# Optimization experiments

Measured on AMD Instinct MI355X. Metric: run time of the kernel, lower is better.

## Reference

```python
import jax, jax.numpy as jnp
import numpy as np

N = 50000      # nodes
E = 800000     # edges
IN = 128       # in_feats
NH = 128       # n_hidden (per-head out_feats)
H = 2          # num_heads
P = 100000     # node pairs for the head MLP
C = 2          # n_classes
NEG_SLOPE = 0.2


def setup_inputs() -> dict:
    key = jax.random.key(0)
    ks = jax.random.split(key, 16)
    def glorot(k, shape, fan_in):
        return jax.random.normal(k, shape, jnp.float32) * (1.0 / np.sqrt(fan_in))
    return {
        "src": jax.random.randint(ks[0], (E,), 0, N),
        "dst": jax.random.randint(ks[1], (E,), 0, N),
        "h": jax.random.normal(ks[2], (N, IN), jnp.float32),
        "x1": jax.random.randint(ks[3], (P,), 0, N),
        "x2": jax.random.randint(ks[4], (P,), 0, N),
        # GATConv layer 0
        "W0": glorot(ks[5], (IN, H * NH), IN),
        "al0": glorot(ks[6], (H, NH), NH),
        "ar0": glorot(ks[7], (H, NH), NH),
        # GATConv layer 1
        "W1": glorot(ks[8], (NH, H * NH), NH),
        "al1": glorot(ks[9], (H, NH), NH),
        "ar1": glorot(ks[10], (H, NH), NH),
        # head MLP (weights stored as [in, out])
        "w1": glorot(ks[11], (3 * NH, NH), 3 * NH),
        "b1": jnp.zeros((NH,), jnp.float32),
        "w2": glorot(ks[12], (NH, C), NH),
        "b2": jnp.zeros((C,), jnp.float32),
    }


def gat_conv(h, src, dst, W, al, ar):
    # h: [N, d_in] -> feat: [N, H, F]
    feat = (h @ W).reshape(h.shape[0], H, -1)
    el = jnp.einsum("nhf,hf->nh", feat, al)  # [N, H]
    er = jnp.einsum("nhf,hf->nh", feat, ar)  # [N, H]
    e = jax.nn.leaky_relu(el[src] + er[dst], NEG_SLOPE)  # [E, H]
    # edge softmax segmented by destination node
    emax = jax.ops.segment_max(e, dst, num_segments=N)
    ee = jnp.exp(e - emax[dst])
    denom = jax.ops.segment_sum(ee, dst, num_segments=N)
    alpha = ee / (denom[dst] + 1e-9)                      # [E, H]
    msg = feat[src] * alpha[..., None]                    # [E, H, F]
    out = jax.ops.segment_sum(msg, dst, num_segments=N)   # [N, H, F]
    return jax.nn.relu(out)


def reference(src, dst, h, x1, x2, W0, al0, ar0, W1, al1, ar1, w1, b1, w2, b2):
    h = gat_conv(h, src, dst, W0, al0, ar0).mean(axis=1)  # [N, NH]
    h = gat_conv(h, src, dst, W1, al1, ar1).mean(axis=1)  # [N, NH]
    h1, h2 = h[x1], h[x2]                                 # [P, NH]
    z = jnp.concatenate([h1, h2, jnp.abs(h1 - h2)], axis=1)
    z = jax.nn.relu(z @ w1 + b1)
    return z @ w2 + b2                                    # [P, C]
```

## Files before the change

### kernel.cpp

```cpp
#include <hip/hip_runtime.h>
#include <hip/hip_bf16.h>

#define NN 50000
#define NE 800000
#define NPAIR 100000

typedef unsigned int u32;
typedef unsigned short u16;
typedef __attribute__((ext_vector_type(8))) short short8;
typedef __attribute__((ext_vector_type(4))) float f32x4;

__device__ __forceinline__ float bflo(u32 u) { return __uint_as_float(u << 16); }
__device__ __forceinline__ float bfhi(u32 u) { return __uint_as_float(u & 0xffff0000u); }
__device__ __forceinline__ u32 bfround(float f) {
    u32 u = __float_as_uint(f);
    return (u + 0x7fffu + ((u >> 16) & 1u)) >> 16;
}
__device__ __forceinline__ u32 packbf(float a, float b) {
    return bfround(a) | (bfround(b) << 16);
}

__global__ __launch_bounds__(256) void count_kernel(const int* __restrict__ dst, int* __restrict__ off) {
    int e = blockIdx.x * 256 + threadIdx.x;
    if (e < NE) atomicAdd(&off[dst[e] + 1], 1);
}

__global__ __launch_bounds__(256) void scan1(int* __restrict__ data, int* __restrict__ bsums, int n) {
    int tid = threadIdx.x;
    int i = blockIdx.x * 256 + tid;
    int v = (i < n) ? data[i] : 0;
    #pragma unroll
    for (int d = 1; d < 64; d <<= 1) {
        int t = __shfl_up(v, d);
        if ((tid & 63) >= d) v += t;
    }
    __shared__ int ws[4];
    if ((tid & 63) == 63) ws[tid >> 6] = v;
    __syncthreads();
    int w = tid >> 6;
    if (w > 0) v += ws[0];
    if (w > 1) v += ws[1];
    if (w > 2) v += ws[2];
    if (i < n) data[i] = v;
    if (tid == 255) bsums[blockIdx.x] = v;
}

__global__ __launch_bounds__(256) void scan2(int* __restrict__ bsums, int nb) {
    int tid = threadIdx.x;
    int v = (tid < nb) ? bsums[tid] : 0;
    #pragma unroll
    for (int d = 1; d < 64; d <<= 1) {
        int t = __shfl_up(v, d);
        if ((tid & 63) >= d) v += t;
    }
    __shared__ int ws[4];
    if ((tid & 63) == 63) ws[tid >> 6] = v;
    __syncthreads();
    int w = tid >> 6;
    if (w > 0) v += ws[0];
    if (w > 1) v += ws[1];
    if (w > 2) v += ws[2];
    if (tid < nb) bsums[tid] = v;
}

__global__ __launch_bounds__(256) void scan3(int* __restrict__ data, const int* __restrict__ bsums, int n) {
    int i = blockIdx.x * 256 + threadIdx.x;
    if (i < n && blockIdx.x > 0) data[i] += bsums[blockIdx.x - 1];
}

__global__ __launch_bounds__(256) void fill_kernel(const int* __restrict__ src, const int* __restrict__ dst,
                                                   const int* __restrict__ off,
                                                   int* __restrict__ cursor, int* __restrict__ srcs) {
    int e = blockIdx.x * 256 + threadIdx.x;
    if (e < NE) {
        int d = dst[e];
        int pos = off[d] + atomicAdd(&cursor[d], 1);
        srcs[pos] = src[e];
    }
}

__global__ __launch_bounds__(256) void pack_all(const float* __restrict__ W0, const float* __restrict__ W1,
                                                const float* __restrict__ w1,
                                                u16* __restrict__ w0pg, u16* __restrict__ w1pg,
                                                u16* __restrict__ w1p) {
    int id = blockIdx.x * 256 + threadIdx.x;
    if (id < 65536) {
        const float* W = (id < 32768) ? W0 : W1;
        u16* Wp = (id < 32768) ? w0pg : w1pg;
        int t = id & 32767;
        int k = t >> 8, n = t & 255;
        int kt = k >> 5, kk = k & 31, lg = kk >> 3, j = kk & 7;
        int nt = n >> 4, ln = n & 15;
        int lane = lg * 16 + ln;
        Wp[(((kt * 16 + nt) * 64) + lane) * 8 + j] = (u16)bfround(W[t]);
    } else if (id < 65536 + 49152) {
        int t = id - 65536;
        int k = t >> 7, n = t & 127;
        int kt = k >> 5, kk = k & 31, lg = kk >> 3, j = kk & 7;
        int ct = n >> 4, ln = n & 15;
        int lane = lg * 16 + ln;
        w1p[(((kt * 8 + ct) * 64) + lane) * 8 + j] = (u16)bfround(w1[t]);
    }
}

template<bool ABF16>
__global__ __launch_bounds__(256) void gemm_mfma(const void* __restrict__ Av,
                                                 const u16* __restrict__ Wp,
                                                 const float* __restrict__ al,
                                                 const float* __restrict__ ar,
                                                 u16* __restrict__ C,
                                                 float* __restrict__ att, int nrows) {
    __shared__ u16 sbuf[64 * 264];
    int rbase = blockIdx.x * 64;
    int tid = threadIdx.x;
    if (ABF16) {
        const uint4* A4 = (const uint4*)Av;
        for (int id = tid; id < 64 * 16; id += 256) {
            int r = id >> 4, seg = id & 15;
            int gr = rbase + r;
            uint4 v = make_uint4(0u, 0u, 0u, 0u);
            if (gr < nrows) v = A4[gr * 16 + seg];
            *(uint4*)&sbuf[r * 136 + seg * 8] = v;
        }
    } else {
        const float4* A4 = (const float4*)Av;
        for (int id = tid; id < 64 * 32; id += 256) {
            int r = id >> 5, seg = id & 31;
            int gr = rbase + r;
            float4 v = make_float4(0.f, 0.f, 0.f, 0.f);
            if (gr < nrows) v = A4[gr * 32 + seg];
            uint2 p;
            p.x = packbf(v.x, v.y);
            p.y = packbf(v.z, v.w);
            *(uint2*)&sbuf[r * 136 + seg * 4] = p;
        }
    }
    __syncthreads();
    int l = tid & 63, w = tid >> 6;
    int ln = l & 15, lg = l >> 4;
    f32x4 acc[16];
    #pragma unroll
    for (int nt = 0; nt < 16; ++nt) acc[nt] = (f32x4){0.f, 0.f, 0.f, 0.f};
    const short8* wp = (const short8*)Wp;
    const u16* arow = &sbuf[(w * 16 + ln) * 136 + lg * 8];
    #pragma unroll
    for (int kt = 0; kt < 4; ++kt) {
        short8 a = *(const short8*)&arow[kt * 32];
        #pragma unroll
        for (int nt = 0; nt < 16; ++nt) {
            short8 b = wp[(kt * 16 + nt) * 64 + l];
            acc[nt] = __builtin_amdgcn_mfma_f32_16x16x32_bf16(a, b, acc[nt], 0, 0, 0);
        }
    }
    float alv[16], arv[16];
    #pragma unroll
    for (int nt = 0; nt < 16; ++nt) {
        alv[nt] = al[nt * 16 + ln];
        arv[nt] = ar[nt * 16 + ln];
    }
    #pragma unroll
    for (int r = 0; r < 4; ++r) {
        float pl0 = 0.f, pr0 = 0.f, pl1 = 0.f, pr1 = 0.f;
        #pragma unroll
        for (int nt = 0; nt < 8; ++nt) {
            pl0 += acc[nt][r] * alv[nt];
            pr0 += acc[nt][r] * arv[nt];
            pl1 += acc[nt + 8][r] * alv[nt + 8];
            pr1 += acc[nt + 8][r] * arv[nt + 8];
        }
        #pragma unroll
        for (int m = 1; m < 16; m <<= 1) {
            pl0 += __shfl_xor(pl0, m); pr0 += __shfl_xor(pr0, m);
            pl1 += __shfl_xor(pl1, m); pr1 += __shfl_xor(pr1, m);
        }
        int grow = rbase + w * 16 + lg * 4 + r;
        if (ln == 0 && grow < nrows) {
            att[grow * 4 + 0] = pl0;
            att[grow * 4 + 1] = pl1;
            att[grow * 4 + 2] = pr0;
            att[grow * 4 + 3] = pr1;
        }
    }
    __syncthreads();
    #pragma unroll
    for (int nt = 0; nt < 16; ++nt) {
        int col = nt * 16 + ln;
        #pragma unroll
        for (int r = 0; r < 4; ++r) {
            int row = w * 16 + lg * 4 + r;
            sbuf[row * 264 + col] = (u16)bfround(acc[nt][r]);
        }
    }
    __syncthreads();
    uint4* C4 = (uint4*)C;
    for (int id = tid; id < 64 * 32; id += 256) {
        int r = id >> 5, seg = id & 31;
        int gr = rbase + r;
        if (gr < nrows) C4[gr * 32 + seg] = *(uint4*)&sbuf[r * 264 + seg * 8];
    }
}

__global__ __launch_bounds__(128) void aggregate(const u16* __restrict__ feat,
                                                 const int* __restrict__ off,
                                                 const int* __restrict__ srcs,
                                                 const float* __restrict__ att,
                                                 u16* __restrict__ hout) {
    int v = blockIdx.x * 2 + (threadIdx.x >> 6);
    int lane = threadIdx.x & 63;
    if (v >= NN) return;
    int s = off[v], deg = off[v + 1] - s;
    const float4* att4 = (const float4*)att;
    const uint2* featu2 = (const uint2*)feat;
    uint2* houtu2 = (uint2*)hout;
    float4 av = att4[v];
    float er0 = av.z, er1 = av.w;
    bool h0 = lane < 32;
    float m0 = -1e30f, m1 = -1e30f, d0 = 0.f, d1 = 0.f;
    float a0 = 0.f, a1 = 0.f, a2 = 0.f, a3 = 0.f;
    for (int cb = 0; cb < deg; cb += 64) {
        int k = cb + lane;
        int cn = min(64, deg - cb);
        int u = 0;
        float e0 = -1e30f, e1 = -1e30f;
        if (k < deg) {
            u = srcs[s + k];
            float4 au = att4[u];
            e0 = au.x + er0; e0 = e0 > 0.f ? e0 : 0.2f * e0;
            e1 = au.y + er1; e1 = e1 > 0.f ? e1 : 0.2f * e1;
        }
        float mc0 = e0, mc1 = e1;
        #pragma unroll
        for (int mm = 1; mm < 64; mm <<= 1) {
            mc0 = fmaxf(mc0, __shfl_xor(mc0, mm));
            mc1 = fmaxf(mc1, __shfl_xor(mc1, mm));
        }
        float m0n = fmaxf(m0, mc0), m1n = fmaxf(m1, mc1);
        float f0 = __expf(m0 - m0n), f1 = __expf(m1 - m1n);
        float w0 = (k < deg) ? __expf(e0 - m0n) : 0.f;
        float w1 = (k < deg) ? __expf(e1 - m1n) : 0.f;
        float s0 = w0, s1 = w1;
        #pragma unroll
        for (int mm = 1; mm < 64; mm <<= 1) {
            s0 += __shfl_xor(s0, mm);
            s1 += __shfl_xor(s1, mm);
        }
        d0 = d0 * f0 + s0;
        d1 = d1 * f1 + s1;
        float fa = h0 ? f0 : f1;
        a0 *= fa; a1 *= fa; a2 *= fa; a3 *= fa;
        m0 = m0n; m1 = m1n;
        int k2 = 0;
        for (; k2 + 4 <= cn; k2 += 4) {
            int uu0 = __shfl(u, k2), uu1 = __shfl(u, k2 + 1);
            int uu2 = __shfl(u, k2 + 2), uu3 = __shfl(u, k2 + 3);
            float wa0 = __shfl(w0, k2), wb0 = __shfl(w1, k2);
            float wa1 = __shfl(w0, k2 + 1), wb1 = __shfl(w1, k2 + 1);
            float wa2 = __shfl(w0, k2 + 2), wb2 = __shfl(w1, k2 + 2);
            float wa3 = __shfl(w0, k2 + 3), wb3 = __shfl(w1, k2 + 3);
            float wk0 = h0 ? wa0 : wb0, wk1 = h0 ? wa1 : wb1;
            float wk2 = h0 ? wa2 : wb2, wk3 = h0 ? wa3 : wb3;
            uint2 g0 = featu2[(size_t)uu0 * 64 + lane];
            uint2 g1 = featu2[(size_t)uu1 * 64 + lane];
            uint2 g2 = featu2[(size_t)uu2 * 64 + lane];
            uint2 g3 = featu2[(size_t)uu3 * 64 + lane];
            a0 += wk0 * bflo(g0.x) + wk1 * bflo(g1.x) + wk2 * bflo(g2.x) + wk3 * bflo(g3.x);
            a1 += wk0 * bfhi(g0.x) + wk1 * bfhi(g1.x) + wk2 * bfhi(g2.x) + wk3 * bfhi(g3.x);
            a2 += wk0 * bflo(g0.y) + wk1 * bflo(g1.y) + wk2 * bflo(g2.y) + wk3 * bflo(g3.y);
            a3 += wk0 * bfhi(g0.y) + wk1 * bfhi(g1.y) + wk2 * bfhi(g2.y) + wk3 * bfhi(g3.y);
        }
        for (; k2 < cn; ++k2) {
            int uu = __shfl(u, k2);
            float wa = __shfl(w0, k2), wb = __shfl(w1, k2);
            float wk = h0 ? wa : wb;
            uint2 g = featu2[(size_t)uu * 64 + lane];
            a0 += wk * bflo(g.x); a1 += wk * bfhi(g.x);
            a2 += wk * bflo(g.y); a3 += wk * bfhi(g.y);
        }
    }
    float dh = h0 ? d0 : d1;
    float r = 1.f / (dh + 1e-9f);
    float o0 = fmaxf(a0 * r, 0.f), o1 = fmaxf(a1 * r, 0.f);
    float o2 = fmaxf(a2 * r, 0.f), o3 = fmaxf(a3 * r, 0.f);
    float p0 = __shfl_xor(o0, 32), p1 = __shfl_xor(o1, 32);
    float p2 = __shfl_xor(o2, 32), p3 = __shfl_xor(o3, 32);
    if (h0) {
        uint2 q;
        q.x = packbf(0.5f * (o0 + p0), 0.5f * (o1 + p1));
        q.y = packbf(0.5f * (o2 + p2), 0.5f * (o3 + p3));
        houtu2[(size_t)v * 32 + lane] = q;
    }
}

__global__ __launch_bounds__(256) void mlp_mfma(const u16* __restrict__ hf,
                                                const int* __restrict__ x1,
                                                const int* __restrict__ x2,
                                                const u16* __restrict__ w1p,
                                                const float* __restrict__ b1,
                                                const float* __restrict__ w2,
                                                const float* __restrict__ b2,
                                                float* __restrict__ out) {
    __shared__ u16 z[64][392];
    int pbase = blockIdx.x * 64;
    int tid = threadIdx.x;
    const uint4* hfu4 = (const uint4*)hf;
    for (int id = tid; id < 64 * 16; id += 256) {
        int p = id >> 4, seg = id & 15;
        int gp = pbase + p;
        uint4 v1 = make_uint4(0u, 0u, 0u, 0u), v2 = v1;
        if (gp < NPAIR) {
            v1 = hfu4[x1[gp] * 16 + seg];
            v2 = hfu4[x2[gp] * 16 + seg];
        }
        int c8 = seg << 3;
        *(uint4*)&z[p][c8] = v1;
        *(uint4*)&z[p][128 + c8] = v2;
        uint4 vd;
        vd.x = packbf(fabsf(bflo(v1.x) - bflo(v2.x)), fabsf(bfhi(v1.x) - bfhi(v2.x)));
        vd.y = packbf(fabsf(bflo(v1.y) - bflo(v2.y)), fabsf(bfhi(v1.y) - bfhi(v2.y)));
        vd.z = packbf(fabsf(bflo(v1.z) - bflo(v2.z)), fabsf(bfhi(v1.z) - bfhi(v2.z)));
        vd.w = packbf(fabsf(bflo(v1.w) - bflo(v2.w)), fabsf(bfhi(v1.w) - bfhi(v2.w)));
        *(uint4*)&z[p][256 + c8] = vd;
    }
    __syncthreads();
    int l = tid & 63, w = tid >> 6;
    int lg = l >> 4, ln = l & 15;
    f32x4 acc[8];
    #pragma unroll
    for (int ct = 0; ct < 8; ++ct) acc[ct] = (f32x4){0.f, 0.f, 0.f, 0.f};
    const short8* wp = (const short8*)w1p;
    const u16* zr = &z[w * 16 + ln][lg * 8];
    for (int kt = 0; kt < 12; ++kt) {
        short8 a = *(const short8*)&zr[kt * 32];
        #pragma unroll
        for (int ct = 0; ct < 8; ++ct) {
            short8 b = wp[(kt * 8 + ct) * 64 + l];
            acc[ct] = __builtin_amdgcn_mfma_f32_16x16x32_bf16(a, b, acc[ct], 0, 0, 0);
        }
    }
    float b1v[8], w20[8], w21[8];
    #pragma unroll
    for (int ct = 0; ct < 8; ++ct) {
        int n = ct * 16 + ln;
        b1v[ct] = b1[n];
        w20[ct] = w2[n * 2 + 0];
        w21[ct] = w2[n * 2 + 1];
    }
    float ob0 = b2[0], ob1 = b2[1];
    #pragma unroll
    for (int r = 0; r < 4; ++r) {
        float p0 = 0.f, p1 = 0.f;
        #pragma unroll
        for (int ct = 0; ct < 8; ++ct) {
            float zv = fmaxf(acc[ct][r] + b1v[ct], 0.f);
            p0 += zv * w20[ct]; p1 += zv * w21[ct];
        }
        #pragma unroll
        for (int m = 1; m < 16; m <<= 1) { p0 += __shfl_xor(p0, m); p1 += __shfl_xor(p1, m); }
        int gp = pbase + w * 16 + lg * 4 + r;
        if (ln == 0 && gp < NPAIR) {
            out[gp * 2 + 0] = p0 + ob0;
            out[gp * 2 + 1] = p1 + ob1;
        }
    }
}

extern "C" void kernel_launch(void* const* d_in, const int* in_sizes, int n_in,
                              void* d_out, int out_size, void* d_ws, size_t ws_size,
                              hipStream_t stream) {
    const int*   src = (const int*)d_in[0];
    const int*   dst = (const int*)d_in[1];
    const float* h   = (const float*)d_in[2];
    const int*   x1  = (const int*)d_in[3];
    const int*   x2  = (const int*)d_in[4];
    const float* W0  = (const float*)d_in[5];
    const float* al0 = (const float*)d_in[6];
    const float* ar0 = (const float*)d_in[7];
    const float* W1  = (const float*)d_in[8];
    const float* al1 = (const float*)d_in[9];
    const float* ar1 = (const float*)d_in[10];
    const float* w1  = (const float*)d_in[11];
    const float* b1  = (const float*)d_in[12];
    const float* w2  = (const float*)d_in[13];
    const float* b2  = (const float*)d_in[14];
    float* out = (float*)d_out;

    char* ws = (char*)d_ws;
    size_t o = 0;
    auto alloc = [&](size_t bytes) { size_t r = o; o = (o + bytes + 255) & ~255UL; return r; };
    int* off    = (int*)(ws + alloc((NN + 1) * sizeof(int)));
    int* cursor = (int*)(ws + alloc(NN * sizeof(int)));
    int* bsums  = (int*)(ws + alloc(256 * sizeof(int)));
    int* srcs   = (int*)(ws + alloc(NE * sizeof(int)));
    float* att  = (float*)(ws + alloc((size_t)NN * 4 * sizeof(float)));
    u16* feat   = (u16*)(ws + alloc((size_t)NN * 256 * sizeof(u16)));
    u16* hb0    = (u16*)(ws + alloc((size_t)NN * 128 * sizeof(u16)));
    u16* hb1    = (u16*)(ws + alloc((size_t)NN * 128 * sizeof(u16)));
    u16* w1p    = (u16*)(ws + alloc((size_t)384 * 128 * sizeof(u16)));
    u16* w0pg   = (u16*)(ws + alloc((size_t)128 * 256 * sizeof(u16)));
    u16* w1pg   = (u16*)(ws + alloc((size_t)128 * 256 * sizeof(u16)));

    hipMemsetAsync(off, 0, (NN + 1) * sizeof(int), stream);
    hipMemsetAsync(cursor, 0, NN * sizeof(int), stream);

    int eblocks = (NE + 255) / 256;
    int nscan = NN + 1;
    int nb = (nscan + 255) / 256;
    count_kernel<<<eblocks, 256, 0, stream>>>(dst, off);
    scan1<<<nb, 256, 0, stream>>>(off, bsums, nscan);
    scan2<<<1, 256, 0, stream>>>(bsums, nb);
    scan3<<<nb, 256, 0, stream>>>(off, bsums, nscan);
    fill_kernel<<<eblocks, 256, 0, stream>>>(src, dst, off, cursor, srcs);
    pack_all<<<448, 256, 0, stream>>>(W0, W1, w1, w0pg, w1pg, w1p);

    int gblocks = (NN + 63) / 64;
    gemm_mfma<false><<<gblocks, 256, 0, stream>>>((const void*)h, w0pg, al0, ar0, feat, att, NN);
    aggregate<<<(NN + 1) / 2, 128, 0, stream>>>(feat, off, srcs, att, hb0);
    gemm_mfma<true><<<gblocks, 256, 0, stream>>>((const void*)hb0, w1pg, al1, ar1, feat, att, NN);
    aggregate<<<(NN + 1) / 2, 128, 0, stream>>>(feat, off, srcs, att, hb1);
    mlp_mfma<<<(NPAIR + 63) / 64, 256, 0, stream>>>(hb1, x1, x2, w1p, b1, w2, b2, out);
}
```

Measured before the change: 383.2 us.

## Widen aggregate gathers to 16-byte loads with two edges per wavefront step

The aggregation kernel now has each lane load a uint4 (8 bf16 values) instead of a uint2. The two half-waves each handle a different edge, so one wavefront gathers two neighbor rows per step, and the partial sums are combined with a cross-half shuffle at the end. The block size doubles to 256 threads (4 nodes per block), and zero-degree nodes take an early-exit path. The aim is fewer, wider memory instructions and more edges in flight per wave, at the cost of extra accumulator registers and a final shuffle reduction.

```diff
diff --git a/kernel.cpp b/kernel.cpp
--- a/kernel.cpp
+++ b/kernel.cpp
@@ -200,23 +200,30 @@
     }
 }
 
-__global__ __launch_bounds__(128) void aggregate(const u16* __restrict__ feat,
+__global__ __launch_bounds__(256) void aggregate(const u16* __restrict__ feat,
                                                  const int* __restrict__ off,
                                                  const int* __restrict__ srcs,
                                                  const float* __restrict__ att,
                                                  u16* __restrict__ hout) {
-    int v = blockIdx.x * 2 + (threadIdx.x >> 6);
+    int v = blockIdx.x * 4 + (threadIdx.x >> 6);
     int lane = threadIdx.x & 63;
     if (v >= NN) return;
     int s = off[v], deg = off[v + 1] - s;
     const float4* att4 = (const float4*)att;
-    const uint2* featu2 = (const uint2*)feat;
-    uint2* houtu2 = (uint2*)hout;
+    const uint4* feat4 = (const uint4*)feat;
+    uint4* hout4 = (uint4*)hout;
+    int seg = lane & 31;
+    int halfsel = lane >> 5;
+    int headbit = (lane >> 4) & 1;
+    if (deg == 0) {
+        if (lane < 16) hout4[(size_t)v * 16 + lane] = make_uint4(0u, 0u, 0u, 0u);
+        return;
+    }
     float4 av = att4[v];
     float er0 = av.z, er1 = av.w;
-    bool h0 = lane < 32;
     float m0 = -1e30f, m1 = -1e30f, d0 = 0.f, d1 = 0.f;
-    float a0 = 0.f, a1 = 0.f, a2 = 0.f, a3 = 0.f;
+    float a0 = 0.f, a1 = 0.f, a2 = 0.f, a3 = 0.f, a4 = 0.f, a5 = 0.f, a6 = 0.f, a7 = 0.f;
+
     for (int cb = 0; cb < deg; cb += 64) {
         int k = cb + lane;
         int cn = min(64, deg - cb);
@@ -246,48 +253,72 @@
         }
         d0 = d0 * f0 + s0;
         d1 = d1 * f1 + s1;
-        float fa = h0 ? f0 : f1;
+        float fa = headbit ? f1 : f0;
         a0 *= fa; a1 *= fa; a2 *= fa; a3 *= fa;
+        a4 *= fa; a5 *= fa; a6 *= fa; a7 *= fa;
         m0 = m0n; m1 = m1n;
+
         int k2 = 0;
-        for (; k2 + 4 <= cn; k2 += 4) {
-            int uu0 = __shfl(u, k2), uu1 = __shfl(u, k2 + 1);
-            int uu2 = __shfl(u, k2 + 2), uu3 = __shfl(u, k2 + 3);
-            float wa0 = __shfl(w0, k2), wb0 = __shfl(w1, k2);
-            float wa1 = __shfl(w0, k2 + 1), wb1 = __shfl(w1, k2 + 1);
-            float wa2 = __shfl(w0, k2 + 2), wb2 = __shfl(w1, k2 + 2);
-            float wa3 = __shfl(w0, k2 + 3), wb3 = __shfl(w1, k2 + 3);
-            float wk0 = h0 ? wa0 : wb0, wk1 = h0 ? wa1 : wb1;
-            float wk2 = h0 ? wa2 : wb2, wk3 = h0 ? wa3 : wb3;
-            uint2 g0 = featu2[(size_t)uu0 * 64 + lane];
-            uint2 g1 = featu2[(size_t)uu1 * 64 + lane];
-            uint2 g2 = featu2[(size_t)uu2 * 64 + lane];
-            uint2 g3 = featu2[(size_t)uu3 * 64 + lane];
-            a0 += wk0 * bflo(g0.x) + wk1 * bflo(g1.x) + wk2 * bflo(g2.x) + wk3 * bflo(g3.x);
-            a1 += wk0 * bfhi(g0.x) + wk1 * bfhi(g1.x) + wk2 * bfhi(g2.x) + wk3 * bfhi(g3.x);
-            a2 += wk0 * bflo(g0.y) + wk1 * bflo(g1.y) + wk2 * bflo(g2.y) + wk3 * bflo(g3.y);
-            a3 += wk0 * bfhi(g0.y) + wk1 * bfhi(g1.y) + wk2 * bfhi(g2.y) + wk3 * bfhi(g3.y);
-        }
-        for (; k2 < cn; ++k2) {
-            int uu = __shfl(u, k2);
-            float wa = __shfl(w0, k2), wb = __shfl(w1, k2);
-            float wk = h0 ? wa : wb;
-            uint2 g = featu2[(size_t)uu * 64 + lane];
+        for (; k2 + 8 <= cn; k2 += 8) {
+            int idxA = k2 + halfsel, idxB = k2 + 2 + halfsel;
+            int idxC = k2 + 4 + halfsel, idxD = k2 + 6 + halfsel;
+            int uA = __shfl(u, idxA), uB = __shfl(u, idxB);
+            int uC = __shfl(u, idxC), uD = __shfl(u, idxD);
+            float wA0 = __shfl(w0, idxA), wA1 = __shfl(w1, idxA);
+            float wB0 = __shfl(w0, idxB), wB1 = __shfl(w1, idxB);
+            float wC0 = __shfl(w0, idxC), wC1 = __shfl(w1, idxC);
+            float wD0 = __shfl(w0, idxD), wD1 = __shfl(w1, idxD);
+            float wA = headbit ? wA1 : wA0;
+            float wB = headbit ? wB1 : wB0;
+            float wC = headbit ? wC1 : wC0;
+            float wD = headbit ? wD1 : wD0;
+            uint4 gA = feat4[(size_t)uA * 32 + seg];
+            uint4 gB = feat4[(size_t)uB * 32 + seg];
+            uint4 gC = feat4[(size_t)uC * 32 + seg];
+            uint4 gD = feat4[(size_t)uD * 32 + seg];
+            a0 += wA * bflo(gA.x) + wB * bflo(gB.x) + wC * bflo(gC.x) + wD * bflo(gD.x);
+            a1 += wA * bfhi(gA.x) + wB * bfhi(gB.x) + wC * bfhi(gC.x) + wD * bfhi(gD.x);
+            a2 += wA * bflo(gA.y) + wB * bflo(gB.y) + wC * bflo(gC.y) + wD * bflo(gD.y);
+            a3 += wA * bfhi(gA.y) + wB * bfhi(gB.y) + wC * bfhi(gC.y) + wD * bfhi(gD.y);
+            a4 += wA * bflo(gA.z) + wB * bflo(gB.z) + wC * bflo(gC.z) + wD * bflo(gD.z);
+            a5 += wA * bfhi(gA.z) + wB * bfhi(gB.z) + wC * bfhi(gC.z) + wD * bfhi(gD.z);
+            a6 += wA * bflo(gA.w) + wB * bflo(gB.w) + wC * bflo(gC.w) + wD * bflo(gD.w);
+            a7 += wA * bfhi(gA.w) + wB * bfhi(gB.w) + wC * bfhi(gC.w) + wD * bfhi(gD.w);
+        }
+        for (; k2 < cn; k2 += 2) {
+            int idx = k2 + halfsel;
+            bool ok = idx < cn;
+            int idxc = ok ? idx : 0;
+            int uu = __shfl(u, idxc);
+            float wk0 = __shfl(w0, idxc), wk1 = __shfl(w1, idxc);
+            float wk = headbit ? wk1 : wk0;
+            if (!ok) wk = 0.f;
+            uint4 g = feat4[(size_t)uu * 32 + seg];
             a0 += wk * bflo(g.x); a1 += wk * bfhi(g.x);
             a2 += wk * bflo(g.y); a3 += wk * bfhi(g.y);
-        }
-    }
-    float dh = h0 ? d0 : d1;
+            a4 += wk * bflo(g.z); a5 += wk * bfhi(g.z);
+            a6 += wk * bflo(g.w); a7 += wk * bfhi(g.w);
+        }
+    }
+    a0 += __shfl_xor(a0, 32); a1 += __shfl_xor(a1, 32);
+    a2 += __shfl_xor(a2, 32); a3 += __shfl_xor(a3, 32);
+    a4 += __shfl_xor(a4, 32); a5 += __shfl_xor(a5, 32);
+    a6 += __shfl_xor(a6, 32); a7 += __shfl_xor(a7, 32);
+    float dh = headbit ? d1 : d0;
     float r = 1.f / (dh + 1e-9f);
     float o0 = fmaxf(a0 * r, 0.f), o1 = fmaxf(a1 * r, 0.f);
     float o2 = fmaxf(a2 * r, 0.f), o3 = fmaxf(a3 * r, 0.f);
-    float p0 = __shfl_xor(o0, 32), p1 = __shfl_xor(o1, 32);
-    float p2 = __shfl_xor(o2, 32), p3 = __shfl_xor(o3, 32);
-    if (h0) {
-        uint2 q;
-        q.x = packbf(0.5f * (o0 + p0), 0.5f * (o1 + p1));
-        q.y = packbf(0.5f * (o2 + p2), 0.5f * (o3 + p3));
-        houtu2[(size_t)v * 32 + lane] = q;
+    float o4 = fmaxf(a4 * r, 0.f), o5 = fmaxf(a5 * r, 0.f);
+    float o6 = fmaxf(a6 * r, 0.f), o7 = fmaxf(a7 * r, 0.f);
+    o0 = 0.5f * (o0 + __shfl_xor(o0, 16)); o1 = 0.5f * (o1 + __shfl_xor(o1, 16));
+    o2 = 0.5f * (o2 + __shfl_xor(o2, 16)); o3 = 0.5f * (o3 + __shfl_xor(o3, 16));
+    o4 = 0.5f * (o4 + __shfl_xor(o4, 16)); o5 = 0.5f * (o5 + __shfl_xor(o5, 16));
+    o6 = 0.5f * (o6 + __shfl_xor(o6, 16)); o7 = 0.5f * (o7 + __shfl_xor(o7, 16));
+    if (lane < 16) {
+        uint4 q;
+        q.x = packbf(o0, o1); q.y = packbf(o2, o3);
+        q.z = packbf(o4, o5); q.w = packbf(o6, o7);
+        hout4[(size_t)v * 16 + lane] = q;
     }
 }
 
@@ -414,8 +445,8 @@
 
     int gblocks = (NN + 63) / 64;
     gemm_mfma<false><<<gblocks, 256, 0, stream>>>((const void*)h, w0pg, al0, ar0, feat, att, NN);
-    aggregate<<<(NN + 1) / 2, 128, 0, stream>>>(feat, off, srcs, att, hb0);
+    aggregate<<<(NN + 3) / 4, 256, 0, stream>>>(feat, off, srcs, att, hb0);
     gemm_mfma<true><<<gblocks, 256, 0, stream>>>((const void*)hb0, w1pg, al1, ar1, feat, att, NN);
-    aggregate<<<(NN + 1) / 2, 128, 0, stream>>>(feat, off, srcs, att, hb1);
+    aggregate<<<(NN + 3) / 4, 256, 0, stream>>>(feat, off, srcs, att, hb1);
     mlp_mfma<<<(NPAIR + 63) / 64, 256, 0, stream>>>(hb1, x1, x2, w1p, b1, w2, b2, out);
 }
```

Measured after the change: 390.8 us. Within noise of the previous version (+2.0%).

## Slice feature matrix into 8 column strips and aggregate per strip

Applied to the files above, without the earlier changes.

The GEMM epilogue now writes its output as eight column-sliced arrays, each holding 16 columns per head for every node (64 bytes per node). The aggregation kernel is split so each block handles one slice for four nodes, with eight lanes covering a slice row and eight edges gathered at once, then reduced across lane groups. The smaller per-slice footprint is meant to make the random gathers more cache-friendly and raise parallelism. In exchange, every slice block recomputes the softmax statistics, which is eight times the attention work, and an extra shuffle reduction is needed.

```diff
diff --git a/kernel.cpp b/kernel.cpp
--- a/kernel.cpp
+++ b/kernel.cpp
@@ -193,37 +193,49 @@
     }
     __syncthreads();
     uint4* C4 = (uint4*)C;
-    for (int id = tid; id < 64 * 32; id += 256) {
-        int r = id >> 5, seg = id & 31;
+    for (int id = tid; id < 2048; id += 256) {
+        int pos = id & 3;
+        int r = (id >> 2) & 63;
+        int s = id >> 8;
         int gr = rbase + r;
-        if (gr < nrows) C4[gr * 32 + seg] = *(uint4*)&sbuf[r * 264 + seg * 8];
-    }
-}
-
-__global__ __launch_bounds__(128) void aggregate(const u16* __restrict__ feat,
+        int col = (pos >> 1) * 128 + 16 * s + 8 * (pos & 1);
+        if (gr < nrows) C4[((size_t)s * NN + gr) * 4 + pos] = *(uint4*)&sbuf[r * 264 + col];
+    }
+}
+
+__global__ __launch_bounds__(256) void aggregate(const u16* __restrict__ featS,
                                                  const int* __restrict__ off,
                                                  const int* __restrict__ srcs,
                                                  const float* __restrict__ att,
                                                  u16* __restrict__ hout) {
-    int v = blockIdx.x * 2 + (threadIdx.x >> 6);
+    int b = blockIdx.x;
+    int s = b & 7;
+    int v = (b >> 3) * 4 + (threadIdx.x >> 6);
     int lane = threadIdx.x & 63;
     if (v >= NN) return;
-    int s = off[v], deg = off[v + 1] - s;
+    int st = off[v], deg = off[v + 1] - st;
     const float4* att4 = (const float4*)att;
-    const uint2* featu2 = (const uint2*)feat;
-    uint2* houtu2 = (uint2*)hout;
+    const uint2* fS = (const uint2*)featS;
+    uint2* hbU2 = (uint2*)hout;
+    int j = lane & 7;
+    int g = lane >> 3;
+    bool h1sel = (lane & 4) != 0;
+    if (deg == 0) {
+        if (lane < 4) hbU2[(size_t)v * 32 + s * 4 + lane] = make_uint2(0u, 0u);
+        return;
+    }
     float4 av = att4[v];
     float er0 = av.z, er1 = av.w;
-    bool h0 = lane < 32;
     float m0 = -1e30f, m1 = -1e30f, d0 = 0.f, d1 = 0.f;
     float a0 = 0.f, a1 = 0.f, a2 = 0.f, a3 = 0.f;
+
     for (int cb = 0; cb < deg; cb += 64) {
         int k = cb + lane;
         int cn = min(64, deg - cb);
         int u = 0;
         float e0 = -1e30f, e1 = -1e30f;
         if (k < deg) {
-            u = srcs[s + k];
+            u = srcs[st + k];
             float4 au = att4[u];
             e0 = au.x + er0; e0 = e0 > 0.f ? e0 : 0.2f * e0;
             e1 = au.y + er1; e1 = e1 > 0.f ? e1 : 0.2f * e1;
@@ -246,48 +258,38 @@
         }
         d0 = d0 * f0 + s0;
         d1 = d1 * f1 + s1;
-        float fa = h0 ? f0 : f1;
+        float fa = h1sel ? f1 : f0;
         a0 *= fa; a1 *= fa; a2 *= fa; a3 *= fa;
         m0 = m0n; m1 = m1n;
-        int k2 = 0;
-        for (; k2 + 4 <= cn; k2 += 4) {
-            int uu0 = __shfl(u, k2), uu1 = __shfl(u, k2 + 1);
-            int uu2 = __shfl(u, k2 + 2), uu3 = __shfl(u, k2 + 3);
-            float wa0 = __shfl(w0, k2), wb0 = __shfl(w1, k2);
-            float wa1 = __shfl(w0, k2 + 1), wb1 = __shfl(w1, k2 + 1);
-            float wa2 = __shfl(w0, k2 + 2), wb2 = __shfl(w1, k2 + 2);
-            float wa3 = __shfl(w0, k2 + 3), wb3 = __shfl(w1, k2 + 3);
-            float wk0 = h0 ? wa0 : wb0, wk1 = h0 ? wa1 : wb1;
-            float wk2 = h0 ? wa2 : wb2, wk3 = h0 ? wa3 : wb3;
-            uint2 g0 = featu2[(size_t)uu0 * 64 + lane];
-            uint2 g1 = featu2[(size_t)uu1 * 64 + lane];
-            uint2 g2 = featu2[(size_t)uu2 * 64 + lane];
-            uint2 g3 = featu2[(size_t)uu3 * 64 + lane];
-            a0 += wk0 * bflo(g0.x) + wk1 * bflo(g1.x) + wk2 * bflo(g2.x) + wk3 * bflo(g3.x);
-            a1 += wk0 * bfhi(g0.x) + wk1 * bfhi(g1.x) + wk2 * bfhi(g2.x) + wk3 * bfhi(g3.x);
-            a2 += wk0 * bflo(g0.y) + wk1 * bflo(g1.y) + wk2 * bflo(g2.y) + wk3 * bflo(g3.y);
-            a3 += wk0 * bfhi(g0.y) + wk1 * bfhi(g1.y) + wk2 * bfhi(g2.y) + wk3 * bfhi(g3.y);
-        }
-        for (; k2 < cn; ++k2) {
-            int uu = __shfl(u, k2);
-            float wa = __shfl(w0, k2), wb = __shfl(w1, k2);
-            float wk = h0 ? wa : wb;
-            uint2 g = featu2[(size_t)uu * 64 + lane];
-            a0 += wk * bflo(g.x); a1 += wk * bfhi(g.x);
-            a2 += wk * bflo(g.y); a3 += wk * bfhi(g.y);
-        }
-    }
-    float dh = h0 ? d0 : d1;
-    float r = 1.f / (dh + 1e-9f);
-    float o0 = fmaxf(a0 * r, 0.f), o1 = fmaxf(a1 * r, 0.f);
-    float o2 = fmaxf(a2 * r, 0.f), o3 = fmaxf(a3 * r, 0.f);
-    float p0 = __shfl_xor(o0, 32), p1 = __shfl_xor(o1, 32);
-    float p2 = __shfl_xor(o2, 32), p3 = __shfl_xor(o3, 32);
-    if (h0) {
+
+        #pragma unroll 2
+        for (int base = 0; base < cn; base += 8) {
+            int idx = base + g;
+            int uu = __shfl(u, idx);
+            float q0 = __shfl(w0, idx), q1 = __shfl(w1, idx);
+            float q = h1sel ? q1 : q0;
+            uint2 gv = fS[((size_t)s * NN + uu) * 8 + j];
+            a0 += q * bflo(gv.x); a1 += q * bfhi(gv.x);
+            a2 += q * bflo(gv.y); a3 += q * bfhi(gv.y);
+        }
+    }
+    a0 += __shfl_xor(a0, 8);  a1 += __shfl_xor(a1, 8);
+    a2 += __shfl_xor(a2, 8);  a3 += __shfl_xor(a3, 8);
+    a0 += __shfl_xor(a0, 16); a1 += __shfl_xor(a1, 16);
+    a2 += __shfl_xor(a2, 16); a3 += __shfl_xor(a3, 16);
+    a0 += __shfl_xor(a0, 32); a1 += __shfl_xor(a1, 32);
+    a2 += __shfl_xor(a2, 32); a3 += __shfl_xor(a3, 32);
+    float r0 = 1.f / (d0 + 1e-9f), r1 = 1.f / (d1 + 1e-9f);
+    float rr = h1sel ? r1 : r0;
+    float o0 = fmaxf(a0 * rr, 0.f), o1 = fmaxf(a1 * rr, 0.f);
+    float o2 = fmaxf(a2 * rr, 0.f), o3 = fmaxf(a3 * rr, 0.f);
+    float p0 = __shfl_xor(o0, 4), p1 = __shfl_xor(o1, 4);
+    float p2 = __shfl_xor(o2, 4), p3 = __shfl_xor(o3, 4);
+    if (lane < 4) {
         uint2 q;
         q.x = packbf(0.5f * (o0 + p0), 0.5f * (o1 + p1));
         q.y = packbf(0.5f * (o2 + p2), 0.5f * (o3 + p3));
-        houtu2[(size_t)v * 32 + lane] = q;
+        hbU2[(size_t)v * 32 + s * 4 + lane] = q;
     }
 }
 
@@ -392,7 +394,7 @@
     int* bsums  = (int*)(ws + alloc(256 * sizeof(int)));
     int* srcs   = (int*)(ws + alloc(NE * sizeof(int)));
     float* att  = (float*)(ws + alloc((size_t)NN * 4 * sizeof(float)));
-    u16* feat   = (u16*)(ws + alloc((size_t)NN * 256 * sizeof(u16)));
+    u16* featS  = (u16*)(ws + alloc((size_t)NN * 256 * sizeof(u16)));
     u16* hb0    = (u16*)(ws + alloc((size_t)NN * 128 * sizeof(u16)));
     u16* hb1    = (u16*)(ws + alloc((size_t)NN * 128 * sizeof(u16)));
     u16* w1p    = (u16*)(ws + alloc((size_t)384 * 128 * sizeof(u16)));
@@ -413,9 +415,10 @@
     pack_all<<<448, 256, 0, stream>>>(W0, W1, w1, w0pg, w1pg, w1p);
 
     int gblocks = (NN + 63) / 64;
-    gemm_mfma<false><<<gblocks, 256, 0, stream>>>((const void*)h, w0pg, al0, ar0, feat, att, NN);
-    aggregate<<<(NN + 1) / 2, 128, 0, stream>>>(feat, off, srcs, att, hb0);
-    gemm_mfma<true><<<gblocks, 256, 0, stream>>>((const void*)hb0, w1pg, al1, ar1, feat, att, NN);
-    aggregate<<<(NN + 1) / 2, 128, 0, stream>>>(feat, off, srcs, att, hb1);
+    int ablocks = ((NN + 3) / 4) * 8;
+    gemm_mfma<false><<<gblocks, 256, 0, stream>>>((const void*)h, w0pg, al0, ar0, featS, att, NN);
+    aggregate<<<ablocks, 256, 0, stream>>>(featS, off, srcs, att, hb0);
+    gemm_mfma<true><<<gblocks, 256, 0, stream>>>((const void*)hb0, w1pg, al1, ar1, featS, att, NN);
+    aggregate<<<ablocks, 256, 0, stream>>>(featS, off, srcs, att, hb1);
     mlp_mfma<<<(NPAIR + 63) / 64, 256, 0, stream>>>(hb1, x1, x2, w1p, b1, w2, b2, out);
 }
```

Result: slower. 657.3 us (+71.5%).
